# Kernel tuning notes

Measured on AMD Instinct MI355X. Metric: run time of the kernel, lower is better.

Reference implementation:

```python
import jax, jax.numpy as jnp
import numpy as np

HEAD = 8
K_DIM = 64
ROUNDS = 4
BUCKETS = 32
ACN = 1  # attend_chunk_num
SELF_VAL = -100000.0


def across(x, acn=ACN):
    """Concatenate each chunk with its acn left/right neighbor chunks (wrapping).
    x: (..., n_chunks, chunk_size, feat). Rolls along chunk axis (-3), cats along -2.
    Order matches the torch code: left chunks, self, right chunks."""
    shifts = list(range(acn, 0, -1)) + [0] + list(range(-1, -acn - 1, -1))
    return jnp.concatenate([jnp.roll(x, s, axis=-3) for s in shifts], axis=-2)


def gather_seq(src, idx):
    """src: (b,h,s,f); idx: (b,h,r,s) -> (b,h,r,s,f) (per-round permutation gather)."""
    return jnp.take_along_axis(src[:, :, None, :, :], idx[..., None], axis=-2)


def lsh_forward(x, Wq, bq, Wv, bv, Wo, bo, hash_vec):
    b, s, d = x.shape
    h, k, r = HEAD, K_DIM, ROUNDS
    qk = (x @ Wq + bq).reshape(b, s, h, k).transpose(0, 2, 1, 3)  # (b,h,s,k)
    v = (x @ Wv + bv).reshape(b, s, h, k).transpose(0, 2, 1, 3)   # (b,h,s,k)

    # --- LSH hashing: argmax over [-rot, rot] rotations ---
    rot = jnp.einsum('bhsk,hkvr->bhsvr', qk, hash_vec)
    rot = jnp.concatenate([-rot, rot], axis=-2)
    buckets = jnp.argmax(rot, axis=-2).transpose(0, 1, 3, 2)  # (b,h,r,s)

    ticker = jnp.arange(s)
    buckets = buckets * s + ticker  # stable-sort key: bucket major, position minor
    s_ticker = jnp.argsort(buckets, axis=-1)
    s_buckets = jnp.take_along_axis(buckets, s_ticker, axis=-1)
    undo = jnp.argsort(s_ticker, axis=-1)

    s_qk = gather_seq(qk, s_ticker)  # (b,h,r,s,k)
    s_v = gather_seq(v, s_ticker)
    nrm = jnp.maximum(jnp.linalg.norm(s_qk, axis=-1, keepdims=True), 1e-12)
    s_k = s_qk / nrm  # F.normalize(p=2)

    nb = BUCKETS
    cs = s // nb
    cq = s_qk.reshape(b, h, r, nb, cs, k)
    ck = s_k.reshape(b, h, r, nb, cs, k)
    cv = s_v.reshape(b, h, r, nb, cs, k)
    ct = s_ticker.reshape(b, h, r, nb, cs)

    ak = across(ck)                      # (b,h,r,nb,3cs,k)
    av = across(cv)
    at = across(ct[..., None])[..., 0]   # (b,h,r,nb,3cs)

    dots = jnp.einsum('bhrnik,bhrnjk->bhrnij', cq, ak) * (k ** -0.5)
    NEG = -jnp.finfo(dots.dtype).max

    # self-attention penalty mask
    dots = jnp.where(ct[..., :, None] == at[..., None, :], SELF_VAL, dots)

    # different-bucket mask
    bid = (s_buckets // s).reshape(b, h, r, nb, cs)
    abid = across(bid[..., None])[..., 0]
    dots = jnp.where(bid[..., :, None] != abid[..., None, :], NEG, dots)

    # duplicate count across rounds (same bucket id in any round)
    loc = (buckets // s).transpose(0, 1, 3, 2)     # (b,h,s,r)
    s_loc = gather_seq(loc, s_ticker)              # (b,h,r,s,r)
    cl = s_loc.reshape(b, h, r, nb, cs, r)
    al = across(cl)                                # (b,h,r,nb,3cs,r)
    dup = (cl[..., :, None, :] == al[..., None, :, :]).sum(-1).astype(dots.dtype)
    dup = jax.lax.stop_gradient(dup)
    dots = dots - jnp.log(dup + 1e-9)

    lse = jax.nn.logsumexp(dots, axis=-1, keepdims=True)
    p = jnp.exp(dots - lse)
    vo = jnp.einsum('bhrnij,bhrnjk->bhrnik', p, av).reshape(b, h, r, s, k)
    lse = lse.reshape(b, h, r, s)

    # unsort back to original token order
    vo = jnp.take_along_axis(vo, undo[..., None], axis=-2)
    lse = jnp.take_along_axis(lse, undo, axis=-1)

    # combine rounds with softmax over per-round logsumexp
    w = jnp.exp(lse - jax.nn.logsumexp(lse, axis=2, keepdims=True))
    out = (vo * w[..., None]).sum(axis=2)  # (b,h,s,k)
    out = out.transpose(0, 2, 1, 3).reshape(b, s, h * k)
    return out @ Wo + bo  # dropout is identity in eval


def setup_inputs() -> dict:
    key = jax.random.key(0)
    ks = jax.random.split(key, 8)
    b, s, d = 2, 2048, 512
    sc = 1.0 / np.sqrt(d)  # keep activations numerically tame
    return {
        'x': jax.random.normal(ks[0], (b, s, d), jnp.float32),
        'Wq': jax.random.normal(ks[1], (d, d), jnp.float32) * sc,
        'bq': jax.random.normal(ks[2], (d,), jnp.float32) * 0.01,
        'Wv': jax.random.normal(ks[3], (d, d), jnp.float32) * sc,
        'bv': jax.random.normal(ks[4], (d,), jnp.float32) * 0.01,
        'Wo': jax.random.normal(ks[5], (d, d), jnp.float32) * sc,
        'bo': jax.random.normal(ks[6], (d,), jnp.float32) * 0.01,
        'hash_vec': jax.random.normal(ks[7], (HEAD, K_DIM, BUCKETS // 2, ROUNDS), jnp.float32),
    }


def reference(x, Wq, bq, Wv, bv, Wo, bo, hash_vec):
    return lsh_forward(x, Wq, bq, Wv, bv, Wo, bo, hash_vec)
```

## Files before the change

kernel.cpp:

```cpp
#include <hip/hip_runtime.h>
#include <hip/hip_bf16.h>
#include <math.h>

#define WS_ 192
#define NEGF (-3.402823466e+38f)

typedef __attribute__((ext_vector_type(8))) short short8;
typedef __attribute__((ext_vector_type(4))) float f32x4;
typedef __attribute__((ext_vector_type(4))) unsigned int u32x4;

static __device__ __forceinline__ unsigned int f2bf(float f) {
    unsigned int u = __float_as_uint(f);
    return (u + 0x7FFFu + ((u >> 16) & 1u)) >> 16;
}
static __device__ __forceinline__ unsigned int packsplit(float v) {
    unsigned int h = f2bf(v);
    float hf = __uint_as_float(h << 16);
    unsigned int l = f2bf(v - hf);
    return h | (l << 16);
}
static __device__ __forceinline__ void mkfrag(uint4 a, uint4 b, short8 &h, short8 &l) {
    u32x4 hv, lv;
    hv[0] = __builtin_amdgcn_perm(a.y, a.x, 0x05040100u);
    hv[1] = __builtin_amdgcn_perm(a.w, a.z, 0x05040100u);
    hv[2] = __builtin_amdgcn_perm(b.y, b.x, 0x05040100u);
    hv[3] = __builtin_amdgcn_perm(b.w, b.z, 0x05040100u);
    lv[0] = __builtin_amdgcn_perm(a.y, a.x, 0x07060302u);
    lv[1] = __builtin_amdgcn_perm(a.w, a.z, 0x07060302u);
    lv[2] = __builtin_amdgcn_perm(b.y, b.x, 0x07060302u);
    lv[3] = __builtin_amdgcn_perm(b.w, b.z, 0x07060302u);
    h = __builtin_bit_cast(short8, hv);
    l = __builtin_bit_cast(short8, lv);
}
static __device__ __forceinline__ unsigned int cvtpk(float lo, float hi) {
    unsigned int d;
    asm("v_cvt_pk_bf16_f32 %0, %1, %2" : "=v"(d) : "v"(lo), "v"(hi));
    return d;
}
static __device__ __forceinline__ void gload_lds16(const void* g, void* l) {
    __builtin_amdgcn_global_load_lds(
        (const __attribute__((address_space(1))) void*)g,
        (__attribute__((address_space(3))) void*)l, 16, 0, 0);
}

__global__ __launch_bounds__(256) void pack_kernel(const float* __restrict__ x,
                                                   const float* __restrict__ Wv,
                                                   const float* __restrict__ Wo,
                                                   unsigned int* __restrict__ xpk,
                                                   unsigned int* __restrict__ wvT,
                                                   unsigned int* __restrict__ woT) {
    __shared__ unsigned int T[64][65];
    const int bid = blockIdx.x;
    const int tid = threadIdx.x;
    if (bid < 2048) {
        int idx = (bid * 256 + tid) * 4;
        float4 v = *(const float4*)(x + idx);
        uint4 pk = make_uint4(packsplit(v.x), packsplit(v.y), packsplit(v.z), packsplit(v.w));
        *(uint4*)(xpk + idx) = pk;
        return;
    }
    int wb = bid - 2048;
    const float* Wsrc = (wb < 64) ? Wv : Wo;
    unsigned int* Wdst = (wb < 64) ? wvT : woT;
    int t = wb & 63;
    int k0 = (t >> 3) * 64, n0 = (t & 7) * 64;
#pragma unroll
    for (int pass = 0; pass < 16; ++pass) {
        int i = pass * 4 + (tid >> 6);
        int j = tid & 63;
        T[j][i] = packsplit(Wsrc[(size_t)(k0 + i) * 512 + n0 + j]);
    }
    __syncthreads();
#pragma unroll
    for (int pass = 0; pass < 16; ++pass) {
        int j = pass * 4 + (tid >> 6);
        int i = tid & 63;
        Wdst[(size_t)(n0 + j) * 512 + k0 + i] = T[j][i];
    }
}

__global__ __launch_bounds__(256) void gemm_qk_hash(const float* __restrict__ A,
                                                    const float* __restrict__ W,
                                                    const float* __restrict__ bias,
                                                    const float* __restrict__ hv,
                                                    unsigned int* __restrict__ Cpk,
                                                    float* __restrict__ scaleQ,
                                                    int* __restrict__ loc2) {
    __shared__ float BUF[4352];
    float* As = BUF;
    float* Ws = BUF + 2176;
    const int m0 = blockIdx.x * 64;
    const int n0 = blockIdx.y * 64;
    const int tid = threadIdx.x;
    const int ty = tid >> 4, tx = tid & 15;
    const int ci = tid & 7, ri = tid >> 3;
    const int wk = tid >> 4, wt = tid & 15;
    float acc[4][4] = {};
    for (int k0 = 0; k0 < 512; k0 += 32) {
#pragma unroll
        for (int h2 = 0; h2 < 2; ++h2) {
            int i = ri + h2 * 32;
            float4 a4 = *(const float4*)(A + (size_t)(m0 + i) * 512 + k0 + ci * 4);
            As[(ci * 4 + 0) * 68 + i] = a4.x;
            As[(ci * 4 + 1) * 68 + i] = a4.y;
            As[(ci * 4 + 2) * 68 + i] = a4.z;
            As[(ci * 4 + 3) * 68 + i] = a4.w;
        }
#pragma unroll
        for (int h2 = 0; h2 < 2; ++h2) {
            int kk = wk + h2 * 16;
            float4 w4 = *(const float4*)(W + (size_t)(k0 + kk) * 512 + n0 + wt * 4);
            *(float4*)(&Ws[kk * 68 + wt * 4]) = w4;
        }
        __syncthreads();
#pragma unroll
        for (int kk = 0; kk < 32; ++kk) {
            float4 a4 = *(float4*)(&As[kk * 68 + ty * 4]);
            float4 w4 = *(float4*)(&Ws[kk * 68 + tx * 4]);
            float a[4] = {a4.x, a4.y, a4.z, a4.w};
            float w[4] = {w4.x, w4.y, w4.z, w4.w};
#pragma unroll
            for (int i = 0; i < 4; ++i)
#pragma unroll
                for (int j = 0; j < 4; ++j) acc[i][j] += a[i] * w[j];
        }
        __syncthreads();
    }
    const int hh = n0 >> 6;
#pragma unroll
    for (int i = 0; i < 4; ++i) {
        int m = m0 + ty * 4 + i;
        int b = m >> 11, s = m & 2047;
        float v0 = acc[i][0] + bias[n0 + tx * 4 + 0];
        float v1 = acc[i][1] + bias[n0 + tx * 4 + 1];
        float v2 = acc[i][2] + bias[n0 + tx * 4 + 2];
        float v3 = acc[i][3] + bias[n0 + tx * 4 + 3];
        acc[i][0] = v0; acc[i][1] = v1; acc[i][2] = v2; acc[i][3] = v3;
        size_t base = ((size_t)(((b << 3) + hh) * 2048 + s)) * 64 + tx * 4;
        uint4 pk = make_uint4(packsplit(v0), packsplit(v1), packsplit(v2), packsplit(v3));
        *(uint4*)(Cpk + base) = pk;
        float sq = v0 * v0 + v1 * v1 + v2 * v2 + v3 * v3;
        sq += __shfl_xor(sq, 1, 16); sq += __shfl_xor(sq, 2, 16);
        sq += __shfl_xor(sq, 4, 16); sq += __shfl_xor(sq, 8, 16);
        if (tx == 0)
            scaleQ[(size_t)(((b << 3) + hh) * 2048 + s)] = 0.125f / fmaxf(sqrtf(sq), 1e-12f);
    }
#pragma unroll
    for (int j = 0; j < 4; ++j) {
        int f = tx * 4 + j;
        int xm = (f & 7) << 3;
#pragma unroll
        for (int i = 0; i < 4; ++i)
            BUF[f * 68 + ((ty * 4 + i) ^ xm)] = acc[i][j];
    }
    __syncthreads();
    const float* hvb = hv + (size_t)hh * 4096 + tx * 4;
    float rt[4][4] = {};
#pragma unroll 4
    for (int f = 0; f < 64; ++f) {
        float4 q4 = *(float4*)(&BUF[f * 68 + ((ty * 4) ^ ((f & 7) << 3))]);
        float4 h4 = *(const float4*)(hvb + f * 64);
        float q[4] = {q4.x, q4.y, q4.z, q4.w};
        float hw[4] = {h4.x, h4.y, h4.z, h4.w};
#pragma unroll
        for (int i = 0; i < 4; ++i)
#pragma unroll
            for (int j = 0; j < 4; ++j) rt[i][j] += q[i] * hw[j];
    }
    __syncthreads();
#pragma unroll
    for (int i = 0; i < 4; ++i)
        *(float4*)(&BUF[(ty * 4 + i) * 68 + tx * 4]) =
            make_float4(rt[i][0], rt[i][1], rt[i][2], rt[i][3]);
    __syncthreads();
    {
        const int tok = tid >> 2, rr2 = tid & 3;
        float best = -BUF[tok * 68 + rr2];
        int bj = 0;
        for (int j = 1; j < 16; ++j) {
            float v = BUF[tok * 68 + j * 4 + rr2];
            if (-v > best) { best = -v; bj = j; }
        }
        for (int j = 0; j < 16; ++j) {
            float v = BUF[tok * 68 + j * 4 + rr2];
            if (v > best) { best = v; bj = 16 + j; }
        }
        int m = m0 + tok;
        int b = m >> 11, s = m & 2047;
        loc2[((size_t)(((b << 3) + hh) * 2048 + s)) * 4 + rr2] = bj;
    }
}

__global__ __launch_bounds__(256) void gemm_pk(const unsigned int* __restrict__ Apk,
                                               const unsigned int* __restrict__ BT,
                                               const float* __restrict__ bias,
                                               void* __restrict__ Cout, int mode) {
    __shared__ __align__(16) unsigned int As[64 * 32];
    __shared__ __align__(16) unsigned int Bs[64 * 32];
    const int m0 = blockIdx.x * 64;
    const int n0 = blockIdx.y * 64;
    const int tid = threadIdx.x;
    const int lane = tid & 63, wv = tid >> 6;
    const int lx = lane & 15, hi = lane >> 4;
    const int wbase = tid & ~63;
    f32x4 acc[4] = {{0.f,0.f,0.f,0.f},{0.f,0.f,0.f,0.f},{0.f,0.f,0.f,0.f},{0.f,0.f,0.f,0.f}};
    for (int k0 = 0; k0 < 512; k0 += 32) {
#pragma unroll
        for (int u = 0; u < 2; ++u) {
            int qi = u * 256 + tid;
            int row = qi >> 3, qd = qi & 7;
            int sq = (qd ^ (row & 7)) << 2;
            gload_lds16(Apk + (size_t)(m0 + row) * 512 + k0 + sq,
                        &As[(u * 256 + wbase) * 4]);
            gload_lds16(BT + (size_t)(n0 + row) * 512 + k0 + sq,
                        &Bs[(u * 256 + wbase) * 4]);
        }
        __syncthreads();
        int arow = wv * 16 + lx;
        uint4 a0 = *(uint4*)(&As[arow * 32 + (((2 * hi) ^ (arow & 7)) << 2)]);
        uint4 a1 = *(uint4*)(&As[arow * 32 + (((2 * hi + 1) ^ (arow & 7)) << 2)]);
        short8 Ah, Al; mkfrag(a0, a1, Ah, Al);
#pragma unroll
        for (int j = 0; j < 4; ++j) {
            int brow = j * 16 + lx;
            uint4 b0 = *(uint4*)(&Bs[brow * 32 + (((2 * hi) ^ (brow & 7)) << 2)]);
            uint4 b1 = *(uint4*)(&Bs[brow * 32 + (((2 * hi + 1) ^ (brow & 7)) << 2)]);
            short8 Bh2, Bl2; mkfrag(b0, b1, Bh2, Bl2);
            acc[j] = __builtin_amdgcn_mfma_f32_16x16x32_bf16(Ah, Bh2, acc[j], 0, 0, 0);
            acc[j] = __builtin_amdgcn_mfma_f32_16x16x32_bf16(Ah, Bl2, acc[j], 0, 0, 0);
            acc[j] = __builtin_amdgcn_mfma_f32_16x16x32_bf16(Al, Bh2, acc[j], 0, 0, 0);
        }
        __syncthreads();
    }
#pragma unroll
    for (int j = 0; j < 4; ++j) {
        int nn = n0 + j * 16 + lx;
        float bs = bias[nn];
#pragma unroll
        for (int reg = 0; reg < 4; ++reg) {
            int m = m0 + wv * 16 + hi * 4 + reg;
            float val = acc[j][reg] + bs;
            if (mode == 0) {
                int b = m >> 11, ss = m & 2047;
                int hh = nn >> 6, f = nn & 63;
                ((unsigned short*)Cout)[((size_t)(((b << 3) + hh) * 2048 + ss)) * 64 + f] =
                    (unsigned short)f2bf(val);
            } else {
                ((float*)Cout)[(size_t)m * 512 + nn] = val;
            }
        }
    }
}

__global__ __launch_bounds__(1024) void sort_kernel(const int* __restrict__ loc2,
                                                    int* __restrict__ st) {
    __shared__ int hist[32][32];
    __shared__ int off[32][32];
    __shared__ int base[32];
    const int gid = blockIdx.x;
    const int r = gid & 3, bh = gid >> 2;
    const int tid = threadIdx.x;
    const int lane = tid & 63, wvi = tid >> 6;
    const unsigned long long lower_mask =
        (lane == 0) ? 0ull : ((~0ull) >> (64 - lane));

    int myb[2], myrank[2];
#pragma unroll
    for (int si = 0; si < 2; ++si) {
        int seg = wvi * 2 + si;
        int p = seg * 64 + lane;
        int b = loc2[(size_t)(bh * 2048 + p) * 4 + r];
        myb[si] = b;
        myrank[si] = 0;
#pragma unroll 1
        for (int bkt = 0; bkt < 32; ++bkt) {
            unsigned long long m = __ballot(b == bkt);
            if (b == bkt) myrank[si] = __popcll(m & lower_mask);
            if (lane == bkt) hist[seg][bkt] = __popcll(m);
        }
    }
    __syncthreads();
    if (tid < 32) {
        int running = 0;
#pragma unroll 1
        for (int seg = 0; seg < 32; ++seg) {
            off[seg][tid] = running;
            running += hist[seg][tid];
        }
        base[tid] = running;
    }
    __syncthreads();
    if (tid == 0) {
        int acc = 0;
#pragma unroll 1
        for (int b = 0; b < 32; ++b) { int h = base[b]; base[b] = acc; acc += h; }
    }
    __syncthreads();
#pragma unroll
    for (int si = 0; si < 2; ++si) {
        int seg = wvi * 2 + si;
        int p = seg * 64 + lane;
        int b = myb[si];
        st[(size_t)gid * 2048 + base[b] + off[seg][b] + myrank[si]] = p;
    }
}

#define KQUAD(row, qd) (((row) << 6) + ((((qd) ^ ((row) & 15))) << 2))
#define PBASE 6400

__global__ __launch_bounds__(256, 3) void attn_kernel(const unsigned int* __restrict__ qkpk,
                                                      const unsigned short* __restrict__ vpk,
                                                      const float* __restrict__ scaleQ,
                                                      const int* __restrict__ loc2,
                                                      const int* __restrict__ st,
                                                      float* __restrict__ lseg,
                                                      float* __restrict__ vog) {
    __shared__ __align__(16) unsigned int U[12800];
    __shared__ float scaleK[WS_];
    __shared__ int Tk[WS_];
    __shared__ int Lp[WS_];

    const int gid = blockIdx.x;
    const int n = gid & 31;
    const int r = (gid >> 5) & 3;
    const int bh = gid >> 7;
    const int tid = threadIdx.x;
    const int sbase = (bh * 4 + r) * 2048;
    const int lane = tid & 63;
    const int wv = tid >> 6;
    const int lx = lane & 15;
    const int hi = lane >> 4;

    if (tid < WS_) {
        int w = tid;
        int chunk = (n + 31 + (w >> 6)) & 31;
        int t = st[(size_t)sbase + chunk * 64 + (w & 63)];
        Tk[w] = t;
        int4 l4 = *(const int4*)(loc2 + (size_t)(bh * 2048 + t) * 4);
        Lp[w] = l4.x | (l4.y << 8) | (l4.z << 16) | (l4.w << 24);
        scaleK[w] = scaleQ[bh * 2048 + t];
    }
    __syncthreads();

    const int fs = tid & 15, wsb = tid >> 4;
#pragma unroll
    for (int it = 0; it < 12; ++it) {
        int row = it * 16 + wsb;
        uint4 v4 = *(const uint4*)(qkpk + ((size_t)(bh * 2048 + Tk[row])) * 64 + fs * 4);
        *(uint4*)(&U[KQUAD(row, fs)]) = v4;
    }
    __syncthreads();

    const int qw = 64 + wv * 16 + lx;
    short8 Bh[2], Bl[2];
#pragma unroll
    for (int ks = 0; ks < 2; ++ks) {
        int qd0 = ks * 8 + hi * 2;
        uint4 a = *(const uint4*)(&U[KQUAD(qw, qd0)]);
        uint4 b = *(const uint4*)(&U[KQUAD(qw, qd0 + 1)]);
        mkfrag(a, b, Bh[ks], Bl[ks]);
    }
    f32x4 s[12];
    __builtin_amdgcn_s_setprio(1);
#pragma unroll
    for (int ct = 0; ct < 12; ++ct) {
        f32x4 acc = {0.f, 0.f, 0.f, 0.f};
#pragma unroll
        for (int ks = 0; ks < 2; ++ks) {
            int arow = ct * 16 + lx;
            int qd0 = ks * 8 + hi * 2;
            uint4 a = *(const uint4*)(&U[KQUAD(arow, qd0)]);
            uint4 b = *(const uint4*)(&U[KQUAD(arow, qd0 + 1)]);
            short8 Ah, Al; mkfrag(a, b, Ah, Al);
            acc = __builtin_amdgcn_mfma_f32_16x16x32_bf16(Ah, Bh[ks], acc, 0, 0, 0);
            acc = __builtin_amdgcn_mfma_f32_16x16x32_bf16(Ah, Bl[ks], acc, 0, 0, 0);
            acc = __builtin_amdgcn_mfma_f32_16x16x32_bf16(Al, Bh[ks], acc, 0, 0, 0);
        }
        s[ct] = acc;
    }
    __builtin_amdgcn_s_setprio(0);

    uint4 vl0[3], vl1[3];
#pragma unroll
    for (int it = 0; it < 3; ++it) {
        int idx = it * 256 + tid;
        int pr = idx >> 3, oct = idx & 7;
        vl0[it] = *(const uint4*)(vpk + ((size_t)(bh * 2048 + Tk[pr * 2])) * 64 + oct * 8);
        vl1[it] = *(const uint4*)(vpk + ((size_t)(bh * 2048 + Tk[pr * 2 + 1])) * 64 + oct * 8);
    }
    __syncthreads();

    const int lq = Lp[qw];
    const unsigned int bmask = 0x80u << (r * 8);
    float mx = -3.0e38f;
#pragma unroll
    for (int ct = 0; ct < 12; ++ct) {
#pragma unroll
        for (int rr = 0; rr < 4; ++rr) {
            int c = ct * 16 + hi * 4 + rr;
            float val = s[ct][rr] * scaleK[c];
            unsigned int x = (unsigned int)(lq ^ Lp[c]);
            unsigned int z = ((x & 0x7f7f7f7fu) + 0x7f7f7f7fu) | x;
            unsigned int zm = ~z & 0x80808080u;
            int dup = __popc(zm);
            val = (c == qw) ? -100000.0f : val;
            val = (zm & bmask) ? val : NEGF;
            float ld = (dup < 2) ? 0.0f
                     : (dup == 2) ? 0.69314718f
                     : (dup == 3) ? 1.09861229f : 1.38629436f;
            val -= ld;
            s[ct][rr] = val;
            mx = fmaxf(mx, val);
        }
    }
    mx = fmaxf(mx, __shfl_xor(mx, 16));
    mx = fmaxf(mx, __shfl_xor(mx, 32));
    float ssum = 0.f;
#pragma unroll
    for (int ct = 0; ct < 12; ++ct)
#pragma unroll
        for (int rr = 0; rr < 4; ++rr) {
            float e = __expf(s[ct][rr] - mx);
            s[ct][rr] = e;
            ssum += e;
        }
    ssum += __shfl_xor(ssum, 16);
    ssum += __shfl_xor(ssum, 32);
    float lse = mx + __logf(ssum);
    if (hi == 0) lseg[(size_t)sbase + Tk[qw]] = lse;
    float inv = 1.0f / ssum;

#pragma unroll
    for (int it = 0; it < 3; ++it) {
        int idx = it * 256 + tid;
        int pr = idx >> 3, oct = idx & 7;
        int c0 = pr * 2;
        unsigned int aw[4] = {vl0[it].x, vl0[it].y, vl0[it].z, vl0[it].w};
        unsigned int bw[4] = {vl1[it].x, vl1[it].y, vl1[it].z, vl1[it].w};
#pragma unroll
        for (int j = 0; j < 8; ++j) {
            int f = oct * 8 + j;
            unsigned int w2 = (j & 1)
                ? __builtin_amdgcn_perm(bw[j >> 1], aw[j >> 1], 0x07060302u)
                : __builtin_amdgcn_perm(bw[j >> 1], aw[j >> 1], 0x05040100u);
            int quad = (c0 >> 3) ^ (f & 7) ^ (f >> 3);
            U[f * 100 + (quad << 2) + ((c0 & 7) >> 1)] = w2;
        }
    }
    const int q = wv * 16 + lx;
    const int pxm = (q & 3) << 3;
#pragma unroll
    for (int ct = 0; ct < 12; ++ct) {
        int po = ct * 8 + hi * 2;
        U[PBASE + q * 100 + ((po + 0) ^ pxm)] = cvtpk(s[ct][0] * inv, s[ct][1] * inv);
        U[PBASE + q * 100 + ((po + 1) ^ pxm)] = cvtpk(s[ct][2] * inv, s[ct][3] * inv);
    }
    __syncthreads();

    f32x4 o[4] = {{0.f,0.f,0.f,0.f},{0.f,0.f,0.f,0.f},{0.f,0.f,0.f,0.f},{0.f,0.f,0.f,0.f}};
    const unsigned short* Uh = (const unsigned short*)U;
    __builtin_amdgcn_s_setprio(1);
#pragma unroll
    for (int ks = 0; ks < 6; ++ks) {
        short8 P8 = *(const short8*)(Uh + PBASE * 2 + q * 200 +
                                     (((ks * 16 + hi * 4) ^ pxm) << 1));
#pragma unroll
        for (int ft = 0; ft < 4; ++ft) {
            int f = ft * 16 + lx;
            int quad = (4 * ks + hi) ^ (f & 7) ^ (f >> 3);
            short8 V8 = *(const short8*)(Uh + f * 200 + (quad << 3));
            o[ft] = __builtin_amdgcn_mfma_f32_16x16x32_bf16(V8, P8, o[ft], 0, 0, 0);
        }
    }
    __builtin_amdgcn_s_setprio(0);
    const int tko = Tk[qw];
#pragma unroll
    for (int ft = 0; ft < 4; ++ft) {
        float4 w4 = make_float4(o[ft][0], o[ft][1], o[ft][2], o[ft][3]);
        *(float4*)(vog + ((size_t)sbase + tko) * 64 + ft * 16 + hi * 4) = w4;
    }
}

__global__ __launch_bounds__(256) void combine_kernel(const float* __restrict__ vog,
                                                      const float* __restrict__ lseg,
                                                      unsigned int* __restrict__ attpk) {
    const int gid = blockIdx.x * 256 + threadIdx.x;
    const int kq = gid & 15;
    const int t = (gid >> 4) & 2047;
    const int bh = gid >> 15;
    const int b = bh >> 3, h = bh & 7;
    float l[4];
    float4 vo[4];
#pragma unroll
    for (int r = 0; r < 4; ++r) {
        l[r] = lseg[(size_t)(bh * 4 + r) * 2048 + t];
        vo[r] = *(const float4*)(vog + ((size_t)(bh * 4 + r) * 2048 + t) * 64 + kq * 4);
    }
    float m = fmaxf(fmaxf(l[0], l[1]), fmaxf(l[2], l[3]));
    float ss = expf(l[0] - m) + expf(l[1] - m) + expf(l[2] - m) + expf(l[3] - m);
    float lt = m + logf(ss);
    float o0 = 0.f, o1 = 0.f, o2 = 0.f, o3 = 0.f;
#pragma unroll
    for (int r = 0; r < 4; ++r) {
        float w = expf(l[r] - lt);
        o0 += w * vo[r].x; o1 += w * vo[r].y; o2 += w * vo[r].z; o3 += w * vo[r].w;
    }
    uint4 pk = make_uint4(packsplit(o0), packsplit(o1), packsplit(o2), packsplit(o3));
    *(uint4*)(attpk + ((size_t)(b * 2048 + t)) * 512 + h * 64 + kq * 4) = pk;
}

extern "C" void kernel_launch(void* const* d_in, const int* in_sizes, int n_in,
                              void* d_out, int out_size, void* d_ws, size_t ws_size,
                              hipStream_t stream) {
    const float* x  = (const float*)d_in[0];
    const float* Wq = (const float*)d_in[1];
    const float* bq = (const float*)d_in[2];
    const float* Wv = (const float*)d_in[3];
    const float* bv = (const float*)d_in[4];
    const float* Wo = (const float*)d_in[5];
    const float* bo = (const float*)d_in[6];
    const float* hv = (const float*)d_in[7];

    unsigned int* W = (unsigned int*)d_ws;
    float*          vog    = (float*)W;
    unsigned int*   xpk    = W + 2097152;
    unsigned int*   qkpk   = W + 8388608;
    unsigned short* vpk    = (unsigned short*)(W + 10485760);
    unsigned int*   attpk  = W + 11534336;
    float*          scaleQ = (float*)(W + 13631488);
    int*            loc2   = (int*)(W + 13664256);
    int*            stbuf  = (int*)(W + 13795328);
    float*          lseg   = (float*)(W + 13926400);
    unsigned int*   wvT    = W + 14057472;
    unsigned int*   woT    = W + 14319616;

    dim3 gg(64, 8), blk(256);
    pack_kernel<<<2176, 256, 0, stream>>>(x, Wv, Wo, xpk, wvT, woT);
    gemm_qk_hash<<<gg, blk, 0, stream>>>(x, Wq, bq, hv, qkpk, scaleQ, loc2);
    gemm_pk<<<gg, blk, 0, stream>>>(xpk, wvT, bv, (void*)vpk, 0);
    sort_kernel<<<64, 1024, 0, stream>>>(loc2, stbuf);
    attn_kernel<<<2048, 256, 0, stream>>>(qkpk, vpk, scaleQ, loc2, stbuf, lseg, vog);
    combine_kernel<<<2048, 256, 0, stream>>>(vog, lseg, attpk);
    gemm_pk<<<gg, blk, 0, stream>>>(attpk, woT, bo, d_out, 1);
}
```

Baseline: 147.5 us.

## Fuse pack and QK GEMM kernels; store QK as split hi/lo bf16 planes

Merges the input/weight packing kernel and the QK projection+hash kernel into one launch, with block indices selecting the role. The QK output is written as separate high and low bf16 halves per row, so the attention kernel can load MFMA fragments directly from LDS without perm-based unpacking. This removes one kernel launch and the per-fragment repacking work in attention. Heterogeneous blocks in one grid may load-balance unevenly, and the QK GEMM blocks now share a launch with the lighter packing blocks.

```diff
diff --git a/kernel.cpp b/kernel.cpp
--- a/kernel.cpp
+++ b/kernel.cpp
@@ -43,55 +43,58 @@
         (__attribute__((address_space(3))) void*)l, 16, 0, 0);
 }
 
-__global__ __launch_bounds__(256) void pack_kernel(const float* __restrict__ x,
+__global__ __launch_bounds__(256) void prep_kernel(const float* __restrict__ A,
+                                                   const float* __restrict__ W,
+                                                   const float* __restrict__ bias,
+                                                   const float* __restrict__ hv,
                                                    const float* __restrict__ Wv,
                                                    const float* __restrict__ Wo,
+                                                   unsigned short* __restrict__ qkr,
+                                                   float* __restrict__ scaleQ,
+                                                   int* __restrict__ loc2,
                                                    unsigned int* __restrict__ xpk,
                                                    unsigned int* __restrict__ wvT,
                                                    unsigned int* __restrict__ woT) {
-    __shared__ unsigned int T[64][65];
+    __shared__ float BUF[4352];
     const int bid = blockIdx.x;
     const int tid = threadIdx.x;
-    if (bid < 2048) {
-        int idx = (bid * 256 + tid) * 4;
-        float4 v = *(const float4*)(x + idx);
-        uint4 pk = make_uint4(packsplit(v.x), packsplit(v.y), packsplit(v.z), packsplit(v.w));
-        *(uint4*)(xpk + idx) = pk;
+
+    if (bid >= 512) {
+        int pb = bid - 512;
+        if (pb < 2048) {
+            int idx = (pb * 256 + tid) * 4;
+            float4 v = *(const float4*)(A + idx);
+            uint4 pk = make_uint4(packsplit(v.x), packsplit(v.y),
+                                  packsplit(v.z), packsplit(v.w));
+            *(uint4*)(xpk + idx) = pk;
+            return;
+        }
+        unsigned int* T = (unsigned int*)BUF;
+        int wb = pb - 2048;
+        const float* Wsrc = (wb < 64) ? Wv : Wo;
+        unsigned int* Wdst = (wb < 64) ? wvT : woT;
+        int t = wb & 63;
+        int k0 = (t >> 3) * 64, n0 = (t & 7) * 64;
+#pragma unroll
+        for (int pass = 0; pass < 16; ++pass) {
+            int i = pass * 4 + (tid >> 6);
+            int j = tid & 63;
+            T[j * 65 + i] = packsplit(Wsrc[(size_t)(k0 + i) * 512 + n0 + j]);
+        }
+        __syncthreads();
+#pragma unroll
+        for (int pass = 0; pass < 16; ++pass) {
+            int j = pass * 4 + (tid >> 6);
+            int i = tid & 63;
+            Wdst[(size_t)(n0 + j) * 512 + k0 + i] = T[j * 65 + i];
+        }
         return;
     }
-    int wb = bid - 2048;
-    const float* Wsrc = (wb < 64) ? Wv : Wo;
-    unsigned int* Wdst = (wb < 64) ? wvT : woT;
-    int t = wb & 63;
-    int k0 = (t >> 3) * 64, n0 = (t & 7) * 64;
-#pragma unroll
-    for (int pass = 0; pass < 16; ++pass) {
-        int i = pass * 4 + (tid >> 6);
-        int j = tid & 63;
-        T[j][i] = packsplit(Wsrc[(size_t)(k0 + i) * 512 + n0 + j]);
-    }
-    __syncthreads();
-#pragma unroll
-    for (int pass = 0; pass < 16; ++pass) {
-        int j = pass * 4 + (tid >> 6);
-        int i = tid & 63;
-        Wdst[(size_t)(n0 + j) * 512 + k0 + i] = T[j][i];
-    }
-}
-
-__global__ __launch_bounds__(256) void gemm_qk_hash(const float* __restrict__ A,
-                                                    const float* __restrict__ W,
-                                                    const float* __restrict__ bias,
-                                                    const float* __restrict__ hv,
-                                                    unsigned int* __restrict__ Cpk,
-                                                    float* __restrict__ scaleQ,
-                                                    int* __restrict__ loc2) {
-    __shared__ float BUF[4352];
+
     float* As = BUF;
     float* Ws = BUF + 2176;
-    const int m0 = blockIdx.x * 64;
-    const int n0 = blockIdx.y * 64;
-    const int tid = threadIdx.x;
+    const int m0 = (bid & 63) * 64;
+    const int n0 = (bid >> 6) * 64;
     const int ty = tid >> 4, tx = tid & 15;
     const int ci = tid & 7, ri = tid >> 3;
     const int wk = tid >> 4, wt = tid & 15;
@@ -136,9 +139,16 @@
         float v2 = acc[i][2] + bias[n0 + tx * 4 + 2];
         float v3 = acc[i][3] + bias[n0 + tx * 4 + 3];
         acc[i][0] = v0; acc[i][1] = v1; acc[i][2] = v2; acc[i][3] = v3;
-        size_t base = ((size_t)(((b << 3) + hh) * 2048 + s)) * 64 + tx * 4;
-        uint4 pk = make_uint4(packsplit(v0), packsplit(v1), packsplit(v2), packsplit(v3));
-        *(uint4*)(Cpk + base) = pk;
+        unsigned int h0 = f2bf(v0), h1 = f2bf(v1), h2v = f2bf(v2), h3 = f2bf(v3);
+        unsigned int l0 = f2bf(v0 - __uint_as_float(h0 << 16));
+        unsigned int l1 = f2bf(v1 - __uint_as_float(h1 << 16));
+        unsigned int l2 = f2bf(v2 - __uint_as_float(h2v << 16));
+        unsigned int l3 = f2bf(v3 - __uint_as_float(h3 << 16));
+        size_t trow = ((size_t)(((b << 3) + hh) * 2048 + s)) * 128;
+        *(uint2*)(qkr + trow + tx * 4) =
+            make_uint2(h0 | (h1 << 16), h2v | (h3 << 16));
+        *(uint2*)(qkr + trow + 64 + tx * 4) =
+            make_uint2(l0 | (l1 << 16), l2 | (l3 << 16));
         float sq = v0 * v0 + v1 * v1 + v2 * v2 + v3 * v3;
         sq += __shfl_xor(sq, 1, 16); sq += __shfl_xor(sq, 2, 16);
         sq += __shfl_xor(sq, 4, 16); sq += __shfl_xor(sq, 8, 16);
@@ -305,10 +315,10 @@
     }
 }
 
-#define KQUAD(row, qd) (((row) << 6) + ((((qd) ^ ((row) & 15))) << 2))
+#define KSLOT(row, sl) (((row) << 6) + ((((sl) ^ ((row) & 15))) << 2))
 #define PBASE 6400
 
-__global__ __launch_bounds__(256, 3) void attn_kernel(const unsigned int* __restrict__ qkpk,
+__global__ __launch_bounds__(256, 3) void attn_kernel(const unsigned short* __restrict__ qkr,
                                                       const unsigned short* __restrict__ vpk,
                                                       const float* __restrict__ scaleQ,
                                                       const int* __restrict__ loc2,
@@ -342,12 +352,12 @@
     }
     __syncthreads();
 
-    const int fs = tid & 15, wsb = tid >> 4;
 #pragma unroll
     for (int it = 0; it < 12; ++it) {
-        int row = it * 16 + wsb;
-        uint4 v4 = *(const uint4*)(qkpk + ((size_t)(bh * 2048 + Tk[row])) * 64 + fs * 4);
-        *(uint4*)(&U[KQUAD(row, fs)]) = v4;
+        int s = it * 256 + tid;
+        int row = s >> 4, sl = s & 15;
+        uint4 v4 = *(const uint4*)(qkr + ((size_t)(bh * 2048 + Tk[row])) * 128 + sl * 8);
+        *(uint4*)(&U[KSLOT(row, sl)]) = v4;
     }
     __syncthreads();
 
@@ -355,10 +365,8 @@
     short8 Bh[2], Bl[2];
 #pragma unroll
     for (int ks = 0; ks < 2; ++ks) {
-        int qd0 = ks * 8 + hi * 2;
-        uint4 a = *(const uint4*)(&U[KQUAD(qw, qd0)]);
-        uint4 b = *(const uint4*)(&U[KQUAD(qw, qd0 + 1)]);
-        mkfrag(a, b, Bh[ks], Bl[ks]);
+        Bh[ks] = __builtin_bit_cast(short8, *(uint4*)(&U[KSLOT(qw, ks * 4 + hi)]));
+        Bl[ks] = __builtin_bit_cast(short8, *(uint4*)(&U[KSLOT(qw, 8 + ks * 4 + hi)]));
     }
     f32x4 s[12];
     __builtin_amdgcn_s_setprio(1);
@@ -368,10 +376,8 @@
 #pragma unroll
         for (int ks = 0; ks < 2; ++ks) {
             int arow = ct * 16 + lx;
-            int qd0 = ks * 8 + hi * 2;
-            uint4 a = *(const uint4*)(&U[KQUAD(arow, qd0)]);
-            uint4 b = *(const uint4*)(&U[KQUAD(arow, qd0 + 1)]);
-            short8 Ah, Al; mkfrag(a, b, Ah, Al);
+            short8 Ah = __builtin_bit_cast(short8, *(uint4*)(&U[KSLOT(arow, ks * 4 + hi)]));
+            short8 Al = __builtin_bit_cast(short8, *(uint4*)(&U[KSLOT(arow, 8 + ks * 4 + hi)]));
             acc = __builtin_amdgcn_mfma_f32_16x16x32_bf16(Ah, Bh[ks], acc, 0, 0, 0);
             acc = __builtin_amdgcn_mfma_f32_16x16x32_bf16(Ah, Bl[ks], acc, 0, 0, 0);
             acc = __builtin_amdgcn_mfma_f32_16x16x32_bf16(Al, Bh[ks], acc, 0, 0, 0);
@@ -524,7 +530,7 @@
     unsigned int* W = (unsigned int*)d_ws;
     float*          vog    = (float*)W;
     unsigned int*   xpk    = W + 2097152;
-    unsigned int*   qkpk   = W + 8388608;
+    unsigned short* qkr    = (unsigned short*)(W + 8388608);
     unsigned short* vpk    = (unsigned short*)(W + 10485760);
     unsigned int*   attpk  = W + 11534336;
     float*          scaleQ = (float*)(W + 13631488);
@@ -535,11 +541,11 @@
     unsigned int*   woT    = W + 14319616;
 
     dim3 gg(64, 8), blk(256);
-    pack_kernel<<<2176, 256, 0, stream>>>(x, Wv, Wo, xpk, wvT, woT);
-    gemm_qk_hash<<<gg, blk, 0, stream>>>(x, Wq, bq, hv, qkpk, scaleQ, loc2);
+    prep_kernel<<<2688, 256, 0, stream>>>(x, Wq, bq, hv, Wv, Wo,
+                                          qkr, scaleQ, loc2, xpk, wvT, woT);
     gemm_pk<<<gg, blk, 0, stream>>>(xpk, wvT, bv, (void*)vpk, 0);
     sort_kernel<<<64, 1024, 0, stream>>>(loc2, stbuf);
-    attn_kernel<<<2048, 256, 0, stream>>>(qkpk, vpk, scaleQ, loc2, stbuf, lseg, vog);
+    attn_kernel<<<2048, 256, 0, stream>>>(qkr, vpk, scaleQ, loc2, stbuf, lseg, vog);
     combine_kernel<<<2048, 256, 0, stream>>>(vog, lseg, attpk);
     gemm_pk<<<gg, blk, 0, stream>>>(attpk, woT, bo, d_out, 1);
 }
```

After: 146.8 us. Within noise of the previous version (-0.5%).
